# Optimization experiments

Measured on AMD Instinct MI355X. Metric: run time of the kernel, lower is better.

Reference implementation:

```python
import jax, jax.numpy as jnp
import numpy as np
import math

B, T, D, H = 2, 2048, 1024, 16
HD = D // H
EPS = 1e-5


def setup_inputs() -> dict:
    key = jax.random.key(0)
    ks = jax.random.split(key, 8)
    s = 0.02
    return {
        "x": jax.random.normal(ks[0], (B, T, D), dtype=jnp.float32),
        "w_attn": jax.random.normal(ks[1], (D, 3 * D), dtype=jnp.float32) * s,
        "w_proj": jax.random.normal(ks[2], (D, D), dtype=jnp.float32) * s,
        "w_fc": jax.random.normal(ks[3], (D, 4 * D), dtype=jnp.float32) * s,
        "w_out": jax.random.normal(ks[4], (4 * D, D), dtype=jnp.float32) * s,
        "ln1_g": jnp.ones((D,), jnp.float32),
        "ln1_b": jnp.zeros((D,), jnp.float32),
        "ln2_g": jnp.ones((D,), jnp.float32),
        "ln2_b": jnp.zeros((D,), jnp.float32),
    }


def _layernorm(x, g, b):
    mu = jnp.mean(x, axis=-1, keepdims=True)
    var = jnp.var(x, axis=-1, keepdims=True)
    return (x - mu) * jax.lax.rsqrt(var + EPS) * g + b


def _attention(x, w_attn, w_proj):
    qkv = x @ w_attn  # [B, T, 3D]
    q, k, v = jnp.split(qkv, 3, axis=-1)
    # [B, H, T, HD]
    q = q.reshape(B, T, H, HD).transpose(0, 2, 1, 3)
    k = k.reshape(B, T, H, HD).transpose(0, 2, 1, 3)
    v = v.reshape(B, T, H, HD).transpose(0, 2, 1, 3)
    att = jnp.einsum('bhqd,bhkd->bhqk', q, k) * (1.0 / math.sqrt(HD))
    causal = jnp.tril(jnp.ones((T, T), dtype=bool))
    att = jnp.where(causal, att, -jnp.inf)
    att = jax.nn.softmax(att, axis=-1)
    y = jnp.einsum('bhqk,bhkd->bhqd', att, v)
    y = y.transpose(0, 2, 1, 3).reshape(B, T, D)
    return y @ w_proj


def reference(x, w_attn, w_proj, w_fc, w_out, ln1_g, ln1_b, ln2_g, ln2_b):
    x = x + _attention(_layernorm(x, ln1_g, ln1_b), w_attn, w_proj)
    h = _layernorm(x, ln2_g, ln2_b)
    h = jax.nn.gelu(h @ w_fc, approximate=False) @ w_out
    return x + h
```

## Files before the change

kernel.cpp:

```cpp
#include <hip/hip_runtime.h>

typedef short s16x8 __attribute__((ext_vector_type(8)));
typedef float f32x4 __attribute__((ext_vector_type(4)));

#define MFMA16(a, b, c) __builtin_amdgcn_mfma_f32_16x16x32_bf16((a), (b), (c), 0, 0, 0)

__device__ __forceinline__ float b2f(unsigned short u) {
    union { unsigned int i; float f; } c;
    c.i = ((unsigned int)u) << 16;
    return c.f;
}
__device__ __forceinline__ unsigned short f2b(float f) {
    union { float f; unsigned int i; } c;
    c.f = f;
    unsigned int i = c.i + 0x7FFFu + ((c.i >> 16) & 1u);
    return (unsigned short)(i >> 16);
}

__device__ __forceinline__ void gl_lds16(const unsigned short* g, unsigned short* l) {
    __builtin_amdgcn_global_load_lds(
        (const __attribute__((address_space(1))) void*)g,
        (__attribute__((address_space(3))) void*)l, 16, 0, 0);
}

__device__ __forceinline__ float gelu_f(float v) {
    float u2 = 1.5957691216057308f * v * (1.0f + 0.044715f * v * v);
    float t = __expf(fminf(u2, 80.0f));
    return v * t * __builtin_amdgcn_rcpf(t + 1.0f);
}

static constexpr size_t OFF_WAT = 0;
static constexpr size_t OFF_WPT = OFF_WAT + 6291456;
static constexpr size_t OFF_WFT = OFF_WPT + 2097152;
static constexpr size_t OFF_WOT = OFF_WFT + 8388608;
static constexpr size_t OFF_R1  = OFF_WOT + 8388608;
static constexpr size_t OFF_R2  = OFF_R1 + 8388608;
static constexpr size_t OFF_VT  = OFF_R2 + 25165824;
static constexpr size_t OFF_Y   = OFF_VT + 8388608;
static constexpr size_t OFF_X2  = OFF_Y + 8388608;

__global__ __launch_bounds__(256) void transpose_all(const float* __restrict__ wA,
                                                     const float* __restrict__ wP,
                                                     const float* __restrict__ wF,
                                                     const float* __restrict__ wO,
                                                     unsigned short* __restrict__ WaT,
                                                     unsigned short* __restrict__ WpT,
                                                     unsigned short* __restrict__ WfT,
                                                     unsigned short* __restrict__ WoT) {
    __shared__ unsigned short tile[32][33];
    const int bb = blockIdx.x;
    const float* W;
    unsigned short* Wt;
    int K, N, rel;
    if (bb < 3072)      { W = wA; Wt = WaT; K = 1024; N = 3072; rel = bb; }
    else if (bb < 4096) { W = wP; Wt = WpT; K = 1024; N = 1024; rel = bb - 3072; }
    else if (bb < 8192) { W = wF; Wt = WfT; K = 1024; N = 4096; rel = bb - 4096; }
    else                { W = wO; Wt = WoT; K = 4096; N = 1024; rel = bb - 8192; }
    const int ntx = N >> 5;
    const int n0 = (rel % ntx) * 32, k0 = (rel / ntx) * 32;
    const int tx = threadIdx.x & 31, ty = threadIdx.x >> 5;
#pragma unroll
    for (int i = 0; i < 32; i += 8)
        tile[ty + i][tx] = f2b(W[(size_t)(k0 + ty + i) * N + (n0 + tx)]);
    __syncthreads();
#pragma unroll
    for (int i = 0; i < 32; i += 8)
        Wt[(size_t)(n0 + ty + i) * K + (k0 + tx)] = tile[tx][ty + i];
}

__global__ __launch_bounds__(256) void ln_kernel(const float* __restrict__ xin,
                                                 const float* __restrict__ gw,
                                                 const float* __restrict__ bw,
                                                 unsigned short* __restrict__ out) {
    const int row = blockIdx.x;
    const int t = threadIdx.x;
    float4 f = ((const float4*)(xin + (size_t)row * 1024))[t];
    float v[4] = {f.x, f.y, f.z, f.w};
    float s = v[0] + v[1] + v[2] + v[3];
    float ss = v[0] * v[0] + v[1] * v[1] + v[2] * v[2] + v[3] * v[3];
#pragma unroll
    for (int o = 32; o >= 1; o >>= 1) {
        s += __shfl_down(s, o);
        ss += __shfl_down(ss, o);
    }
    __shared__ float red[2][4];
    const int wv = t >> 6, ln = t & 63;
    if (ln == 0) { red[0][wv] = s; red[1][wv] = ss; }
    __syncthreads();
    s = red[0][0] + red[0][1] + red[0][2] + red[0][3];
    ss = red[1][0] + red[1][1] + red[1][2] + red[1][3];
    const float mu = s * (1.0f / 1024.0f);
    const float rs = rsqrtf(ss * (1.0f / 1024.0f) - mu * mu + 1e-5f);
    float4 gg = ((const float4*)gw)[t];
    float4 bb = ((const float4*)bw)[t];
    ushort4 o4;
    o4.x = f2b((v[0] - mu) * rs * gg.x + bb.x);
    o4.y = f2b((v[1] - mu) * rs * gg.y + bb.y);
    o4.z = f2b((v[2] - mu) * rs * gg.z + bb.z);
    o4.w = f2b((v[3] - mu) * rs * gg.w + bb.w);
    ((ushort4*)(out + (size_t)row * 1024))[t] = o4;
}

template <int EPI, int BN>
__global__ __launch_bounds__(256) void gemm_bt(const unsigned short* __restrict__ A,
                                               const unsigned short* __restrict__ Bt,
                                               void* __restrict__ outp,
                                               const float* __restrict__ residp,
                                               unsigned short* __restrict__ vtp,
                                               int M, int N, int K) {
    constexpr int NWC = (BN == 128) ? 2 : 1;
    constexpr int AI  = (BN == 128) ? 4 : 2;
    constexpr int PB  = BN / 32;
    __shared__ unsigned short As[128 * 64];
    __shared__ unsigned short Bs[BN * 64];
    const int m0 = blockIdx.y * 128, n0 = blockIdx.x * BN;
    const int tid = threadIdx.x;
    const int w = tid >> 6, lane = tid & 63, quad = lane >> 4, lk = lane & 15;
    const int wr = w / NWC, wc = w % NWC;
    const int lrow = lane >> 3, lchunk = lane & 7;
    const int cg = lchunk ^ (lrow & 7);

    const unsigned short* aP = A + (size_t)(m0 + w * 32 + lrow) * K + cg * 8;
    const unsigned short* bP = Bt + (size_t)(n0 + w * (BN / 4) + lrow) * K + cg * 8;
    unsigned short* lA = As + (w * 32) * 64;
    unsigned short* lB = Bs + (w * (BN / 4)) * 64;

    f32x4 acc[AI][4];
#pragma unroll
    for (int i = 0; i < AI; ++i)
#pragma unroll
        for (int j = 0; j < 4; ++j) acc[i][j] = (f32x4){0.f, 0.f, 0.f, 0.f};

    const int KT = K >> 6;
    for (int kb = 0; kb < KT; ++kb) {
        const unsigned short* aPk = aP + kb * 64;
        const unsigned short* bPk = bP + kb * 64;
#pragma unroll
        for (int p = 0; p < 4; ++p)
            gl_lds16(aPk + (size_t)p * 8 * K, lA + p * 8 * 64);
#pragma unroll
        for (int p = 0; p < PB; ++p)
            gl_lds16(bPk + (size_t)p * 8 * K, lB + p * 8 * 64);
        __syncthreads();
#pragma unroll
        for (int ks = 0; ks < 2; ++ks) {
            const int s = (ks * 4 + quad) ^ (lk & 7);
            s16x8 af[AI], bfv[4];
#pragma unroll
            for (int i = 0; i < AI; ++i)
                af[i] = *(const s16x8*)(As + (wr * (AI * 16) + i * 16 + lk) * 64 + s * 8);
#pragma unroll
            for (int j = 0; j < 4; ++j)
                bfv[j] = *(const s16x8*)(Bs + (wc * 64 + j * 16 + lk) * 64 + s * 8);
#pragma unroll
            for (int i = 0; i < AI; ++i)
#pragma unroll
                for (int j = 0; j < 4; ++j)
                    acc[i][j] = MFMA16(af[i], bfv[j], acc[i][j]);
        }
        __syncthreads();
    }

    const int gr0 = m0 + wr * (AI * 16);
    const int gc0 = n0 + wc * 64;
    if constexpr (EPI == 2) {
#pragma unroll
        for (int i = 0; i < AI; ++i)
#pragma unroll
            for (int r = 0; r < 4; ++r) {
                const int gr = gr0 + i * 16 + quad * 4 + r;
                const size_t ro = (size_t)gr * N;
#pragma unroll
                for (int j = 0; j < 4; ++j) {
                    const int gc = gc0 + j * 16 + lk;
                    ((float*)outp)[ro + gc] = residp[ro + gc] + acc[i][j][r];
                }
            }
    } else if (EPI == 3 && gc0 >= 2048) {
        const int h = (gc0 - 2048) >> 6;
        const int bq = m0 >> 11;
        const size_t vb = (size_t)(bq * 16 + h) * 64;
        const int tg0 = (m0 & 2047) + wr * (AI * 16);
        unsigned short* Ept = As + w * 2048;
#pragma unroll
        for (int i = 0; i < AI; ++i) {
#pragma unroll
            for (int j = 0; j < 4; ++j)
#pragma unroll
                for (int r = 0; r < 4; ++r)
                    Ept[(j * 16 + lk) * 24 + quad * 4 + r] = f2b(acc[i][j][r]);
            const int d = lane;
#pragma unroll
            for (int half = 0; half < 2; ++half) {
                uint4 dd = *(const uint4*)(Ept + d * 24 + half * 8);
                *(uint4*)(vtp + (vb + d) * 2048 + tg0 + i * 16 + half * 8) = dd;
            }
        }
    } else {
        unsigned short* Ep = As + w * (16 * 72);
#pragma unroll
        for (int i = 0; i < AI; ++i) {
#pragma unroll
            for (int j = 0; j < 4; ++j)
#pragma unroll
                for (int r = 0; r < 4; ++r) {
                    float v = acc[i][j][r];
                    if constexpr (EPI == 1) v = gelu_f(v);
                    Ep[(quad * 4 + r) * 72 + j * 16 + lk] = f2b(v);
                }
#pragma unroll
            for (int c = 0; c < 2; ++c) {
                const int row = c * 8 + lrow;
                uint4 d = *(const uint4*)(Ep + row * 72 + lchunk * 8);
                const int gr = gr0 + i * 16 + row;
                *(uint4*)((unsigned short*)outp + (size_t)gr * N + gc0 + lchunk * 8) = d;
            }
        }
    }
}

__global__ __launch_bounds__(256) void attn_kernel(const unsigned short* __restrict__ qkv,
                                                   const unsigned short* __restrict__ vt,
                                                   unsigned short* __restrict__ y) {
    __shared__ unsigned short Ks[64 * 64];
    __shared__ unsigned short Vs[64 * 64];
    __shared__ __align__(16) unsigned short Ps[4][2][576];
    const int tid = threadIdx.x;
    const int w = tid >> 6, lane = tid & 63, quad = lane >> 4, lk = lane & 15;
    const int bb = blockIdx.x;
    const int bh = bb & 31;
    const int p = bb >> 5;
    const int b = bh >> 4, h = bh & 15;
    const size_t rowbase = (size_t)b * 2048;
    const size_t vbase = (size_t)bh * 64;
    const int nt = 32 - p;
    const int rq[2] = {p * 64 + w * 16, (31 - p) * 64 + w * 16};

    const int lrow = lane >> 3, lchunk = lane & 7;

    s16x8 qf[2][2];
#pragma unroll
    for (int si = 0; si < 2; ++si)
#pragma unroll
        for (int ks = 0; ks < 2; ++ks) {
            s16x8 q = *(const s16x8*)(qkv + (rowbase + rq[si] + lk) * 3072 + h * 64 +
                                      ks * 32 + quad * 8);
#pragma unroll
            for (int e = 0; e < 8; ++e) {
                union { unsigned int i; float f; } cc;
                cc.i = ((unsigned int)(unsigned short)q[e]) << 16;
                cc.f *= 0.125f;
                q[e] = (short)(cc.i >> 16);
            }
            qf[si][ks] = q;
        }

    f32x4 oacc[2][4];
    float rsum[2][4];
#pragma unroll
    for (int si = 0; si < 2; ++si) {
#pragma unroll
        for (int dj = 0; dj < 4; ++dj) oacc[si][dj] = (f32x4){0.f, 0.f, 0.f, 0.f};
#pragma unroll
        for (int r = 0; r < 4; ++r) rsum[si][r] = 0.f;
    }

    const int srow = w * 16 + lrow;
    const int cgs = lchunk ^ (srow & 7);
    const unsigned short* kgp = qkv + (rowbase + srow) * 3072 + 1024 + h * 64 + cgs * 8;
    const unsigned short* vgp = vt + (vbase + srow) * 2048 + cgs * 8;
    unsigned short* kl = Ks + w * 1024;
    unsigned short* vl = Vs + w * 1024;

    for (int t = 0; t < nt; ++t) {
#pragma unroll
        for (int i = 0; i < 2; ++i) {
            gl_lds16(kgp + ((size_t)t * 64 + i * 8) * 3072, kl + i * 512);
            gl_lds16(vgp + t * 64 + (size_t)i * 8 * 2048, vl + i * 512);
        }
        __syncthreads();
#pragma unroll
        for (int half = 0; half < 2; ++half) {
            const int k0 = t * 64 + half * 32;
            s16x8 kf[2][2], vf[4];
#pragma unroll
            for (int nj = 0; nj < 2; ++nj)
#pragma unroll
                for (int ks = 0; ks < 2; ++ks) {
                    const int row = half * 32 + nj * 16 + lk;
                    const int s = (ks * 4 + quad) ^ (lk & 7);
                    kf[nj][ks] = *(const s16x8*)(Ks + row * 64 + s * 8);
                }
#pragma unroll
            for (int dj = 0; dj < 4; ++dj) {
                const int s = (half * 4 + quad) ^ (lk & 7);
                vf[dj] = *(const s16x8*)(Vs + (dj * 16 + lk) * 64 + s * 8);
            }
#pragma unroll
            for (int si = 0; si < 2; ++si) {
                const int r0 = rq[si];
                if (k0 > r0 + 15) continue;
                const bool domask = (k0 + 31 > r0);
                f32x4 s[2];
                s[0] = (f32x4){0.f, 0.f, 0.f, 0.f};
                s[1] = (f32x4){0.f, 0.f, 0.f, 0.f};
#pragma unroll
                for (int ks = 0; ks < 2; ++ks) {
                    s[0] = MFMA16(qf[si][ks], kf[0][ks], s[0]);
                    s[1] = MFMA16(qf[si][ks], kf[1][ks], s[1]);
                }
                unsigned short* Pw = Ps[w][si];
#pragma unroll
                for (int nj = 0; nj < 2; ++nj)
#pragma unroll
                    for (int r = 0; r < 4; ++r) {
                        float pv = __expf(s[nj][r]);
                        if (domask) {
                            const int key = k0 + nj * 16 + lk;
                            const int row = r0 + quad * 4 + r;
                            if (key > row) pv = 0.f;
                        }
                        union { float f; unsigned int i; } cc;
                        cc.f = pv;
                        cc.i &= 0xFFFF0000u;
                        rsum[si][r] += cc.f;
                        Pw[(quad * 4 + r) * 36 + nj * 16 + lk] = (unsigned short)(cc.i >> 16);
                    }
                const s16x8 af = *(const s16x8*)(Pw + lk * 36 + quad * 8);
#pragma unroll
                for (int dj = 0; dj < 4; ++dj)
                    oacc[si][dj] = MFMA16(af, vf[dj], oacc[si][dj]);
            }
        }
        __syncthreads();
    }

#pragma unroll
    for (int si = 0; si < 2; ++si) {
#pragma unroll
        for (int o = 1; o < 16; o <<= 1)
#pragma unroll
            for (int r = 0; r < 4; ++r) rsum[si][r] += __shfl_xor(rsum[si][r], o);
        float inv[4];
#pragma unroll
        for (int r = 0; r < 4; ++r) inv[r] = 1.0f / rsum[si][r];
        unsigned short* St = Ps[w][0];
#pragma unroll
        for (int dj = 0; dj < 4; ++dj)
#pragma unroll
            for (int r = 0; r < 4; ++r)
                St[(quad * 4 + r) * 72 + dj * 16 + lk] = f2b(oacc[si][dj][r] * inv[r]);
#pragma unroll
        for (int i = 0; i < 2; ++i) {
            const int row = lane >> 2, chk = (lane & 3) + 4 * i;
            uint4 d = *(const uint4*)(St + row * 72 + chk * 8);
            *(uint4*)(y + (rowbase + rq[si] + row) * 1024 + h * 64 + chk * 8) = d;
        }
    }
}

extern "C" void kernel_launch(void* const* d_in, const int* in_sizes, int n_in,
                              void* d_out, int out_size, void* d_ws, size_t ws_size,
                              hipStream_t stream) {
    const float* x   = (const float*)d_in[0];
    const float* wA  = (const float*)d_in[1];
    const float* wP  = (const float*)d_in[2];
    const float* wF  = (const float*)d_in[3];
    const float* wO  = (const float*)d_in[4];
    const float* g1  = (const float*)d_in[5];
    const float* b1  = (const float*)d_in[6];
    const float* g2  = (const float*)d_in[7];
    const float* b2v = (const float*)d_in[8];

    char* ws = (char*)d_ws;
    unsigned short* WaT  = (unsigned short*)(ws + OFF_WAT);
    unsigned short* WpT  = (unsigned short*)(ws + OFF_WPT);
    unsigned short* WfT  = (unsigned short*)(ws + OFF_WFT);
    unsigned short* WoT  = (unsigned short*)(ws + OFF_WOT);
    unsigned short* xn1  = (unsigned short*)(ws + OFF_R1);
    unsigned short* qkv  = (unsigned short*)(ws + OFF_R2);
    unsigned short* gbuf = (unsigned short*)(ws + OFF_R2);
    unsigned short* vt   = (unsigned short*)(ws + OFF_VT);
    unsigned short* y    = (unsigned short*)(ws + OFF_Y);
    float*          x2   = (float*)(ws + OFF_X2);
    unsigned short* h2   = xn1;
    float*          outf = (float*)d_out;

    transpose_all<<<12288, 256, 0, stream>>>(wA, wP, wF, wO, WaT, WpT, WfT, WoT);
    ln_kernel<<<4096, 256, 0, stream>>>(x, g1, b1, xn1);
    gemm_bt<3, 128><<<dim3(24, 32), 256, 0, stream>>>(xn1, WaT, qkv, nullptr, vt,
                                                      4096, 3072, 1024);
    attn_kernel<<<512, 256, 0, stream>>>(qkv, vt, y);
    gemm_bt<2, 64><<<dim3(16, 32), 256, 0, stream>>>(y, WpT, x2, x, nullptr,
                                                     4096, 1024, 1024);
    ln_kernel<<<4096, 256, 0, stream>>>(x2, g2, b2v, h2);
    gemm_bt<1, 128><<<dim3(32, 32), 256, 0, stream>>>(h2, WfT, gbuf, nullptr, nullptr,
                                                      4096, 4096, 1024);
    gemm_bt<2, 64><<<dim3(16, 32), 256, 0, stream>>>(gbuf, WoT, outf, x2, nullptr,
                                                     4096, 1024, 4096);
}
```

Measured before the change: 330.5 us.

## Split-K the output projection GEMM with atomics and fuse LN1 into weight prep

The final FC-out GEMM (K=4096) is split four ways along K via a grid z-dimension. Each split atomically adds its partial tile into the output, which the second layernorm kernel pre-fills with the residual x2. The first layernorm is folded into the weight transpose/convert kernel as extra blocks, removing one launch. Split-K raises the block count with a wider 128-column tile, at the cost of float atomics on the output and nondeterministic summation order.

```diff
diff --git a/kernel.cpp b/kernel.cpp
--- a/kernel.cpp
+++ b/kernel.cpp
@@ -39,16 +39,50 @@
 static constexpr size_t OFF_Y   = OFF_VT + 8388608;
 static constexpr size_t OFF_X2  = OFF_Y + 8388608;
 
-__global__ __launch_bounds__(256) void transpose_all(const float* __restrict__ wA,
-                                                     const float* __restrict__ wP,
-                                                     const float* __restrict__ wF,
-                                                     const float* __restrict__ wO,
-                                                     unsigned short* __restrict__ WaT,
-                                                     unsigned short* __restrict__ WpT,
-                                                     unsigned short* __restrict__ WfT,
-                                                     unsigned short* __restrict__ WoT) {
+__global__ __launch_bounds__(256) void prep_kernel(const float* __restrict__ wA,
+                                                   const float* __restrict__ wP,
+                                                   const float* __restrict__ wF,
+                                                   const float* __restrict__ wO,
+                                                   unsigned short* __restrict__ WaT,
+                                                   unsigned short* __restrict__ WpT,
+                                                   unsigned short* __restrict__ WfT,
+                                                   unsigned short* __restrict__ WoT,
+                                                   const float* __restrict__ x,
+                                                   const float* __restrict__ g1,
+                                                   const float* __restrict__ b1,
+                                                   unsigned short* __restrict__ xn1) {
     __shared__ unsigned short tile[32][33];
+    __shared__ float red[2][4];
     const int bb = blockIdx.x;
+    if (bb >= 12288) {
+        const int row = bb - 12288;
+        const int t = threadIdx.x;
+        float4 f = ((const float4*)(x + (size_t)row * 1024))[t];
+        float v[4] = {f.x, f.y, f.z, f.w};
+        float s = v[0] + v[1] + v[2] + v[3];
+        float ss = v[0] * v[0] + v[1] * v[1] + v[2] * v[2] + v[3] * v[3];
+#pragma unroll
+        for (int o = 32; o >= 1; o >>= 1) {
+            s += __shfl_down(s, o);
+            ss += __shfl_down(ss, o);
+        }
+        const int wv = t >> 6, ln = t & 63;
+        if (ln == 0) { red[0][wv] = s; red[1][wv] = ss; }
+        __syncthreads();
+        s = red[0][0] + red[0][1] + red[0][2] + red[0][3];
+        ss = red[1][0] + red[1][1] + red[1][2] + red[1][3];
+        const float mu = s * (1.0f / 1024.0f);
+        const float rs = rsqrtf(ss * (1.0f / 1024.0f) - mu * mu + 1e-5f);
+        float4 gg = ((const float4*)g1)[t];
+        float4 bbv = ((const float4*)b1)[t];
+        ushort4 o4;
+        o4.x = f2b((v[0] - mu) * rs * gg.x + bbv.x);
+        o4.y = f2b((v[1] - mu) * rs * gg.y + bbv.y);
+        o4.z = f2b((v[2] - mu) * rs * gg.z + bbv.z);
+        o4.w = f2b((v[3] - mu) * rs * gg.w + bbv.w);
+        ((ushort4*)(xn1 + (size_t)row * 1024))[t] = o4;
+        return;
+    }
     const float* W;
     unsigned short* Wt;
     int K, N, rel;
@@ -71,10 +105,12 @@
 __global__ __launch_bounds__(256) void ln_kernel(const float* __restrict__ xin,
                                                  const float* __restrict__ gw,
                                                  const float* __restrict__ bw,
-                                                 unsigned short* __restrict__ out) {
+                                                 unsigned short* __restrict__ out,
+                                                 float* __restrict__ copyf) {
     const int row = blockIdx.x;
     const int t = threadIdx.x;
     float4 f = ((const float4*)(xin + (size_t)row * 1024))[t];
+    if (copyf) ((float4*)(copyf + (size_t)row * 1024))[t] = f;
     float v[4] = {f.x, f.y, f.z, f.w};
     float s = v[0] + v[1] + v[2] + v[3];
     float ss = v[0] * v[0] + v[1] * v[1] + v[2] * v[2] + v[3] * v[3];
@@ -131,8 +167,9 @@
 #pragma unroll
         for (int j = 0; j < 4; ++j) acc[i][j] = (f32x4){0.f, 0.f, 0.f, 0.f};
 
-    const int KT = K >> 6;
-    for (int kb = 0; kb < KT; ++kb) {
+    const int kb0 = (EPI == 4) ? blockIdx.z * 16 : 0;
+    const int kb1 = (EPI == 4) ? kb0 + 16 : (K >> 6);
+    for (int kb = kb0; kb < kb1; ++kb) {
         const unsigned short* aPk = aP + kb * 64;
         const unsigned short* bPk = bP + kb * 64;
 #pragma unroll
@@ -174,6 +211,19 @@
                 for (int j = 0; j < 4; ++j) {
                     const int gc = gc0 + j * 16 + lk;
                     ((float*)outp)[ro + gc] = residp[ro + gc] + acc[i][j][r];
+                }
+            }
+    } else if constexpr (EPI == 4) {
+#pragma unroll
+        for (int i = 0; i < AI; ++i)
+#pragma unroll
+            for (int r = 0; r < 4; ++r) {
+                const int gr = gr0 + i * 16 + quad * 4 + r;
+                const size_t ro = (size_t)gr * N;
+#pragma unroll
+                for (int j = 0; j < 4; ++j) {
+                    const int gc = gc0 + j * 16 + lk;
+                    unsafeAtomicAdd(&((float*)outp)[ro + gc], acc[i][j][r]);
                 }
             }
     } else if (EPI == 3 && gc0 >= 2048) {
@@ -386,16 +436,16 @@
     unsigned short* h2   = xn1;
     float*          outf = (float*)d_out;
 
-    transpose_all<<<12288, 256, 0, stream>>>(wA, wP, wF, wO, WaT, WpT, WfT, WoT);
-    ln_kernel<<<4096, 256, 0, stream>>>(x, g1, b1, xn1);
+    prep_kernel<<<16384, 256, 0, stream>>>(wA, wP, wF, wO, WaT, WpT, WfT, WoT,
+                                           x, g1, b1, xn1);
     gemm_bt<3, 128><<<dim3(24, 32), 256, 0, stream>>>(xn1, WaT, qkv, nullptr, vt,
                                                       4096, 3072, 1024);
     attn_kernel<<<512, 256, 0, stream>>>(qkv, vt, y);
     gemm_bt<2, 64><<<dim3(16, 32), 256, 0, stream>>>(y, WpT, x2, x, nullptr,
                                                      4096, 1024, 1024);
-    ln_kernel<<<4096, 256, 0, stream>>>(x2, g2, b2v, h2);
+    ln_kernel<<<4096, 256, 0, stream>>>(x2, g2, b2v, h2, outf);
     gemm_bt<1, 128><<<dim3(32, 32), 256, 0, stream>>>(h2, WfT, gbuf, nullptr, nullptr,
                                                       4096, 4096, 1024);
-    gemm_bt<2, 64><<<dim3(16, 32), 256, 0, stream>>>(gbuf, WoT, outf, x2, nullptr,
-                                                     4096, 1024, 4096);
-}
+    gemm_bt<4, 128><<<dim3(8, 32, 4), 256, 0, stream>>>(gbuf, WoT, outf, nullptr, nullptr,
+                                                        4096, 1024, 4096);
+}
```

New measurement: 368.9 us. 1.12x slower.
